# Performance work log

Measured on AMD Instinct MI355X. Metric: run time of the kernel, lower is better.

Reference implementation:

```python
import jax, jax.numpy as jnp
import numpy as np

Hh, Ww, Cc = 8, 8, 16        # observation grid h, w, channels
N = Hh * Ww                  # 64 graph nodes (one per grid cell)
B = 4096                     # batch
HEADS, COUT = 4, 32          # GAT heads, per-head output dim (concat -> 128)
HID, ADIM = 128, 6           # hidden_dim, action_dim
GAT_OUT = N * HEADS * COUT   # 8192 flattened GAT output per sample
NEG = -9e15


def _grid_adj():
    # 4-connected grid graph with self loops (make_graph's static edge structure)
    A = np.zeros((N, N), np.int32)
    for r in range(Hh):
        for c in range(Ww):
            i = r * Ww + c
            A[i, i] = 1
            for dr, dc in ((1, 0), (-1, 0), (0, 1), (0, -1)):
                rr, cc = r + dr, c + dc
                if 0 <= rr < Hh and 0 <= cc < Ww:
                    A[i, rr * Ww + cc] = 1
    return jnp.asarray(A)


def setup_inputs() -> dict:
    key = jax.random.key(0)
    ks = iter(jax.random.split(key, 40))
    p = lambda *s: jax.random.normal(next(ks), s, jnp.float32) * 0.1
    z = lambda *s: jnp.zeros(s, jnp.float32)
    return dict(
        x=jax.random.normal(next(ks), (B, Hh * Ww * Cc), jnp.float32),
        adj=_grid_adj(),
        actor_h=z(B, HID), actor_c=z(B, HID),
        critic_h=z(B, HID), critic_c=z(B, HID),
        gat1_W=p(Cc, HEADS * COUT), gat1_b=z(HEADS * COUT), gat1_a=p(HEADS, 2 * COUT),
        d1_W=p(GAT_OUT, HID), d1_b=z(HID),
        lstm1_Wi=p(HID, 4 * HID), lstm1_Wh=p(HID, 4 * HID), lstm1_b=z(4 * HID),
        ln1_s=jnp.ones((HID,), jnp.float32), ln1_bi=z(HID),
        d2_W=p(HID, HID), d2_b=z(HID),
        d3_W=p(HID, HID), d3_b=z(HID),
        dout_W=p(HID, ADIM), dout_b=z(ADIM),
        gat2_W=p(Cc, HEADS * COUT), gat2_b=z(HEADS * COUT), gat2_a=p(HEADS, 2 * COUT),
        c1_W=p(GAT_OUT, HID), c1_b=z(HID),
        lstm2_Wi=p(HID, 4 * HID), lstm2_Wh=p(HID, 4 * HID), lstm2_b=z(4 * HID),
        ln2_s=jnp.ones((HID,), jnp.float32), ln2_bi=z(HID),
        c2_W=p(HID, HID), c2_b=z(HID),
        c3_W=p(HID, HID), c3_b=z(HID),
        cout_W=p(HID, 1), cout_b=z(1),
    )


def _gat(feats, adj, W, b, a):
    # feats: [B,N,Cc]; adj: [N,N] int; multi-head GAT with concat heads
    h = (feats @ W + b).reshape(B, N, HEADS, COUT)           # [B,N,H,C]
    ls = jnp.einsum('bnhc,hc->bnh', h, a[:, :COUT])          # source logit
    ld = jnp.einsum('bnhc,hc->bnh', h, a[:, COUT:])          # dest logit
    logits = jax.nn.leaky_relu(ls[:, :, None, :] + ld[:, None, :, :], 0.2)  # [B,N,N,H]
    logits = jnp.where(adj[None, :, :, None] > 0, logits, NEG)
    attn = jax.nn.softmax(logits, axis=2)                    # over neighbors
    return jnp.einsum('bnmh,bmhc->bnhc', attn, h).reshape(B, -1)  # [B, N*H*C]


def _lstm(h, c, xin, Wi, Wh, bh):
    # flax OptimizedLSTMCell: gates in order i,f,g,o; bias only on hidden path
    z = xin @ Wi + h @ Wh + bh
    i, f, g, o = jnp.split(z, 4, axis=-1)
    nc = jax.nn.sigmoid(f) * c + jax.nn.sigmoid(i) * jnp.tanh(g)
    nh = jax.nn.sigmoid(o) * jnp.tanh(nc)
    return nh, nc


def _ln(v, s, b):
    mu = v.mean(-1, keepdims=True)
    var = v.var(-1, keepdims=True)
    return (v - mu) * jax.lax.rsqrt(var + 1e-6) * s + b


def reference(x, adj, actor_h, actor_c, critic_h, critic_c,
              gat1_W, gat1_b, gat1_a, d1_W, d1_b,
              lstm1_Wi, lstm1_Wh, lstm1_b, ln1_s, ln1_bi,
              d2_W, d2_b, d3_W, d3_b, dout_W, dout_b,
              gat2_W, gat2_b, gat2_a, c1_W, c1_b,
              lstm2_Wi, lstm2_Wh, lstm2_b, ln2_s, ln2_bi,
              c2_W, c2_b, c3_W, c3_b, cout_W, cout_b):
    act = jnp.tanh
    feats = x.reshape(B, N, Cc)
    # actor branch
    am = act(_gat(feats, adj, gat1_W, gat1_b, gat1_a) @ d1_W + d1_b)
    a_h, a_c = _lstm(actor_h, actor_c, am, lstm1_Wi, lstm1_Wh, lstm1_b)
    am = _ln(a_h, ln1_s, ln1_bi)
    am = act(am @ d2_W + d2_b)
    am = act(am @ d3_W + d3_b)
    logits = am @ dout_W + dout_b                            # Categorical logits
    # critic branch
    cm = act(_gat(feats, adj, gat2_W, gat2_b, gat2_a) @ c1_W + c1_b)
    c_h, c_c = _lstm(critic_h, critic_c, cm, lstm2_Wi, lstm2_Wh, lstm2_b)
    cm = _ln(c_h, ln2_s, ln2_bi)
    cm = act(cm @ c2_W + c2_b)
    cm = act(cm @ c3_W + c3_b)
    value = (cm @ cout_W + cout_b).squeeze(-1)
    return logits, value, a_h, a_c, c_h, c_c
```

## Files before the change

### kernel.cpp

```cpp
#include <hip/hip_runtime.h>
#include <hip/hip_bf16.h>

#define BATCH 4096
#define NN    64
#define CIN   16
#define NHEAD 4
#define CO    32
#define HC    128
#define HID   128
#define ADIM  6
#define K1    8192
#define LDH   136
#define KSPLIT 8

typedef __attribute__((ext_vector_type(8))) short bf16x8;
typedef __attribute__((ext_vector_type(8))) unsigned short u16x8;
typedef __attribute__((ext_vector_type(4))) float f32x4;

__device__ __forceinline__ float bf2f(unsigned short u) {
    unsigned int v = ((unsigned int)u) << 16;
    return __uint_as_float(v);
}
__device__ __forceinline__ unsigned short f2bf(float x) {
    union { __hip_bfloat16 h; unsigned short u; } cv;
    cv.h = __float2bfloat16(x);
    return cv.u;
}
__device__ __forceinline__ float sigmf(float x) { return 1.f / (1.f + expf(-x)); }

__device__ __forceinline__ void gload_lds16(const void* g, void* l) {
    __builtin_amdgcn_global_load_lds(
        (const __attribute__((address_space(1))) unsigned int*)(uintptr_t)g,
        (__attribute__((address_space(3))) unsigned int*)(uintptr_t)l,
        16, 0, 0);
}

struct TJob { const float* in; unsigned short* out; int K; int N; int ldo; };
struct TJobs { TJob j[8]; };

__global__ __launch_bounds__(256) void k_prep(
    const float* __restrict__ d1W, const float* __restrict__ c1W,
    unsigned short* __restrict__ Wt1, unsigned short* __restrict__ Wt2,
    TJobs jobs,
    const float* __restrict__ ha, const float* __restrict__ hc,
    unsigned short* __restrict__ X,
    const int* __restrict__ adj, unsigned long long* __restrict__ masks,
    const float* __restrict__ l1b, const float* __restrict__ l2b,
    const float* __restrict__ b2,  const float* __restrict__ c2b,
    const float* __restrict__ b3,  const float* __restrict__ c3b,
    float* __restrict__ biasz, float* __restrict__ b2p, float* __restrict__ b3p,
    const float* __restrict__ g1W, const float* __restrict__ g2W,
    const float* __restrict__ g1a, const float* __restrict__ g2a,
    const float* __restrict__ g1b, const float* __restrict__ g2b,
    unsigned short* __restrict__ wtg,
    float* __restrict__ blsld)
{
    const int bid = blockIdx.x;
    const int t   = threadIdx.x;

    if (bid < 1024) {
        __shared__ float s[64][33];
        const int  zsel = bid >> 9;
        const float* W  = zsel ? c1W : d1W;
        unsigned short* Wt = zsel ? Wt2 : Wt1;
        const int k0 = (bid & 127) * 64;
        const int n0 = ((bid >> 7) & 3) * 32;
        const int kr = t >> 5, nc = t & 31;
#pragma unroll
        for (int i = 0; i < 8; ++i)
            s[kr + 8 * i][nc] = W[(size_t)(k0 + kr + 8 * i) * HC + n0 + nc];
        __syncthreads();
#pragma unroll
        for (int j = 0; j < 8; ++j) {
            const int idx = j * 256 + t;
            const int n = idx >> 6, k = idx & 63;
            Wt[(size_t)(n0 + n) * K1 + k0 + k] = f2bf(s[k][n]);
        }
    } else if (bid < 1536) {
        const int b   = bid - 1024;
        const int job = b >> 6, idx = b & 63;
        const TJob jb = jobs.j[job];
        const int ntk = jb.K >> 5, ntn = jb.N >> 5;
        if (idx >= ntk * ntn) return;
        const int tk = idx % ntk, tn = idx / ntk;
        __shared__ float s2[32][33];
        const int kr = t >> 5, nc = t & 31;
        const int k0 = tk * 32, n0 = tn * 32;
#pragma unroll
        for (int i = 0; i < 4; ++i)
            s2[kr + 8 * i][nc] = jb.in[(size_t)(k0 + kr + 8 * i) * jb.N + n0 + nc];
        __syncthreads();
#pragma unroll
        for (int i = 0; i < 4; ++i) {
            const int idx2 = i * 256 + t;
            const int n = idx2 >> 5, k = idx2 & 31;
            jb.out[(size_t)(n0 + n) * jb.ldo + k0 + k] = f2bf(s2[k][n]);
        }
    } else if (bid < 2560) {
        const int gid = (bid - 1536) * 256 + t;
        const int zi  = gid >> 17;
        const int rem = gid & 131071;
        const int s3  = rem >> 5, c4 = rem & 31;
        const float4 v = reinterpret_cast<const float4*>(zi ? hc : ha)[(size_t)s3 * 32 + c4];
        ushort4 u;
        u.x = f2bf(v.x); u.y = f2bf(v.y); u.z = f2bf(v.z); u.w = f2bf(v.w);
        reinterpret_cast<ushort4*>(X + (size_t)zi * BATCH * 256 + (size_t)s3 * 256 + 128)[c4] = u;
    } else {
#pragma unroll
        for (int it = 0; it < 4; ++it) {
            const int tt = t + it * 256;
            if (tt < NN) {
                unsigned long long m = 0ull;
                for (int j = 0; j < NN; ++j)
                    if (adj[tt * NN + j] > 0) m |= (1ull << j);
                masks[tt] = m;
            }
            biasz[tt] = (tt < 512) ? l1b[tt] : l2b[tt - 512];
            if (tt < HID) {
                b2p[tt]       = b2[tt];
                b2p[HID + tt] = c2b[tt];
                b3p[tt]       = b3[tt];
                b3p[HID + tt] = c3b[tt];
            }
        }
#pragma unroll
        for (int q = 0; q < 16; ++q) {
            const int idx = t * 16 + q;
            const int set = idx >> 11;
            const int rem = idx & 2047;
            const int col = rem >> 4, k = rem & 15;
            wtg[set * 2304 + col * 16 + k] = f2bf((set ? g2W : g1W)[k * HC + col]);
        }
        {
            const int set = t >> 7, rem = t & 127;
            const int e = rem >> 4, k = rem & 15;
            const float* W  = set ? g2W : g1W;
            const float* aa = set ? g2a : g1a;
            const int hdh = e & 3, off = (e < 4) ? 0 : 32;
            float v = 0.f;
            for (int c = 0; c < 32; ++c)
                v += W[k * HC + hdh * 32 + c] * aa[hdh * 64 + off + c];
            wtg[set * 2304 + (128 + e) * 16 + k] = f2bf(v);
            wtg[set * 2304 + (136 + e) * 16 + k] = 0;
        }
        if (t < 16) {
            const int s2 = t >> 3, e2 = t & 7;
            const float* bb2 = s2 ? g2b : g1b;
            const float* aa2 = s2 ? g2a : g1a;
            const int h2 = e2 & 3, o2 = (e2 < 4) ? 0 : 32;
            float bv = 0.f;
            for (int c = 0; c < 32; ++c)
                bv += bb2[h2 * 32 + c] * aa2[h2 * 64 + o2 + c];
            blsld[s2 * 8 + e2] = bv;
        }
    }
}

struct GatW { const unsigned short* Wt; const float* b; const float* bls; unsigned short* out; };
struct GatArgs { GatW g[2]; };

__global__ __launch_bounds__(256) void k_gat(
    const float* __restrict__ x,
    const unsigned long long* __restrict__ masks,
    GatArgs ga, int zbase)
{
    const GatW gw = ga.g[zbase + blockIdx.y];
    const unsigned short* __restrict__ Wtg = gw.Wt;
    const float* __restrict__ bias = gw.b;
    const float* __restrict__ bls  = gw.bls;
    unsigned short* __restrict__ out = gw.out;

    union UB {
        struct { unsigned short feat[64][16]; unsigned short wt[144][16]; } stg;
        unsigned short P[2][64][72];
    };
    __shared__ UB u;
    __shared__ unsigned short s_hT[128][72];
    __shared__ float s_ls[64][4];
    __shared__ float s_ld[64][4];
    __shared__ float s_bias[HC];
    __shared__ float s_bls[8];
    __shared__ unsigned long long s_mask[NN];

    const int t = threadIdx.x;
    const int b = blockIdx.x;

    {
        const int n = t >> 2, c0 = (t & 3) * 4;
        const float4 v = reinterpret_cast<const float4*>(x + (size_t)b * (NN * CIN))[t];
        ushort4 q;
        q.x = f2bf(v.x); q.y = f2bf(v.y); q.z = f2bf(v.z); q.w = f2bf(v.w);
        *reinterpret_cast<ushort4*>(&u.stg.feat[n][c0]) = q;
        if (t < 144) {
            *reinterpret_cast<u16x8*>(&u.stg.wt[t][0]) = *reinterpret_cast<const u16x8*>(Wtg + t * 16);
            *reinterpret_cast<u16x8*>(&u.stg.wt[t][8]) = *reinterpret_cast<const u16x8*>(Wtg + t * 16 + 8);
        }
        if (t < HC) s_bias[t] = bias[t];
        if (t < 8)  s_bls[t] = bls[t];
        if (t < NN) s_mask[t] = masks[t];
    }
    __syncthreads();

    const int w = t >> 6, lane = t & 63;
    const int row16 = lane & 15;
    const int jr4   = lane >> 4;

    {
        const bool lo = lane < 32;
        const int k0 = (jr4 & 1) * 8;
        const bf16x8 zf = { 0, 0, 0, 0, 0, 0, 0, 0 };
        const bf16x8 aF = lo ? *reinterpret_cast<const bf16x8*>(&u.stg.feat[w * 16 + row16][k0]) : zf;
        bf16x8 bF[9];
#pragma unroll
        for (int ct = 0; ct < 9; ++ct)
            bF[ct] = lo ? *reinterpret_cast<const bf16x8*>(&u.stg.wt[ct * 16 + row16][k0]) : zf;
        f32x4 acc[9] = {};
#pragma unroll
        for (int ct = 0; ct < 9; ++ct)
            acc[ct] = __builtin_amdgcn_mfma_f32_16x16x32_bf16(aF, bF[ct], acc[ct], 0, 0, 0);
#pragma unroll
        for (int ct = 0; ct < 8; ++ct) {
            const int col = ct * 16 + row16;
            const float bv = s_bias[col];
            ushort4 q;
            q.x = f2bf(acc[ct][0] + bv);
            q.y = f2bf(acc[ct][1] + bv);
            q.z = f2bf(acc[ct][2] + bv);
            q.w = f2bf(acc[ct][3] + bv);
            *reinterpret_cast<ushort4*>(&s_hT[col][w * 16 + jr4 * 4]) = q;
        }
        if (row16 < 8) {
            const float bb = s_bls[row16];
#pragma unroll
            for (int j = 0; j < 4; ++j) {
                const int r = w * 16 + jr4 * 4 + j;
                if (row16 < 4) s_ls[r][row16]     = acc[8][j] + bb;
                else           s_ld[r][row16 - 4] = acc[8][j] + bb;
            }
        }
    }
    __syncthreads();

    const int n  = t >> 2;
    const int hd = t & 3;
    float p[5]; int mc[5]; bool ok[5];
    {
        const unsigned long long m = s_mask[n];
        const int cand[5] = { n - 8, n - 1, n, n + 1, n + 8 };
#pragma unroll
        for (int e = 0; e < 5; ++e) {
            const int cm = cand[e];
            const bool inr = (cm >= 0) && (cm < NN);
            mc[e] = inr ? cm : n;
            ok[e] = inr && ((m >> mc[e]) & 1ull);
        }
        const float lsn = s_ls[n][hd];
        float sum = 0.f;
#pragma unroll
        for (int e = 0; e < 5; ++e) {
            float v = lsn + s_ld[mc[e]][hd];
            v = (v > 0.f) ? v : 0.2f * v;
            p[e] = ok[e] ? __expf(v) : 0.f;
            sum += p[e];
        }
        const float inv = 1.f / sum;
#pragma unroll
        for (int e = 0; e < 5; ++e) p[e] *= inv;
    }

    {
        char* pb = (char*)&u.P[0][0][0];
#pragma unroll
        for (int i = 0; i < 9; ++i)
            *reinterpret_cast<unsigned long long*>(pb + t * 72 + i * 8) = 0ull;
    }
    __syncthreads();

    unsigned short* ob = out + (size_t)b * K1;

#pragma unroll
    for (int pass = 0; pass < 2; ++pass) {
        if ((hd >> 1) == pass) {
#pragma unroll
            for (int e = 0; e < 5; ++e)
                if (ok[e]) u.P[hd & 1][n][mc[e]] = f2bf(p[e]);
        }
        __syncthreads();

        const int hh  = pass * 2 + (w >> 1);
        const int ph  = w >> 1;
        const int mtb = (w & 1) * 2;
        f32x4 acc[2][2] = {};
#pragma unroll
        for (int kt = 0; kt < 2; ++kt) {
            const int kof = kt * 32 + jr4 * 8;
            bf16x8 aF[2], bF[2];
#pragma unroll
            for (int mtl = 0; mtl < 2; ++mtl)
                aF[mtl] = *reinterpret_cast<const bf16x8*>(&u.P[ph][(mtb + mtl) * 16 + row16][kof]);
#pragma unroll
            for (int nt = 0; nt < 2; ++nt)
                bF[nt] = *reinterpret_cast<const bf16x8*>(&s_hT[hh * 32 + nt * 16 + row16][kof]);
#pragma unroll
            for (int mtl = 0; mtl < 2; ++mtl)
#pragma unroll
                for (int nt = 0; nt < 2; ++nt)
                    acc[mtl][nt] = __builtin_amdgcn_mfma_f32_16x16x32_bf16(
                        aF[mtl], bF[nt], acc[mtl][nt], 0, 0, 0);
        }
#pragma unroll
        for (int mtl = 0; mtl < 2; ++mtl)
#pragma unroll
            for (int nt = 0; nt < 2; ++nt) {
                const int ch = hh * 32 + nt * 16 + row16;
#pragma unroll
                for (int j = 0; j < 4; ++j) {
                    const int node = (mtb + mtl) * 16 + jr4 * 4 + j;
                    ob[node * HC + ch] = f2bf(acc[mtl][nt][j]);
                }
            }
        if (pass == 0) __syncthreads();
    }
}

__global__ __launch_bounds__(256) void k_mmsk(
    const unsigned short* __restrict__ A0, const unsigned short* __restrict__ A1,
    const unsigned short* __restrict__ Bt0, const unsigned short* __restrict__ Bt1,
    float* __restrict__ accum)
{
    __shared__ unsigned short sbuf[2][160 * 64];

    const int br   = blockIdx.y;
    const unsigned short* A  = br ? A1 : A0;
    const unsigned short* Bt = br ? Bt1 : Bt0;
    float* acc_out = accum + (size_t)br * BATCH * HID;

    const int t    = threadIdx.x;
    const int w    = t >> 6;
    const int lane = t & 63;
    const int m0   = blockIdx.x * 32;
    const int kbase = blockIdx.z * (K1 / KSPLIT);
    const int kiters = (K1 / KSPLIT) / 64;

    const char* srcp[5];
    int ldsoff[5];
#pragma unroll
    for (int q = 0; q < 5; ++q) {
        const int c     = w * 5 + q;
        const int p     = c * 1024 + lane * 16;
        const int prow  = p >> 7;
        const int pslot = (p >> 4) & 7;
        const int lslot = pslot ^ (prow & 7);
        ldsoff[q] = c * 1024;
        if (c < 4)
            srcp[q] = (const char*)(A + (size_t)(m0 + prow) * K1 + kbase + lslot * 8);
        else
            srcp[q] = (const char*)(Bt + (size_t)(prow - 32) * K1 + kbase + lslot * 8);
    }

    f32x4 acc[2][2] = {};

#pragma unroll
    for (int q = 0; q < 5; ++q)
        gload_lds16(srcp[q], (char*)&sbuf[0][0] + ldsoff[q]);
    __syncthreads();

    int buf = 0;
    for (int it = 0; it < kiters; ++it) {
        if (it + 1 < kiters) {
            const size_t kbyte = (size_t)(it + 1) * 128;
#pragma unroll
            for (int q = 0; q < 5; ++q)
                gload_lds16(srcp[q] + kbyte, (char*)&sbuf[buf ^ 1][0] + ldsoff[q]);
        }
        const char* bb = (const char*)&sbuf[buf][0];
        bf16x8 aF[2][2], bF[2][2];
#pragma unroll
        for (int kb = 0; kb < 2; ++kb) {
            const int slot = kb * 4 + (lane >> 4);
#pragma unroll
            for (int rb = 0; rb < 2; ++rb) {
                const int row = rb * 16 + (lane & 15);
                aF[rb][kb] = *(const bf16x8*)(bb + row * 128 + ((slot ^ (row & 7)) << 4));
            }
#pragma unroll
            for (int cb = 0; cb < 2; ++cb) {
                const int row = 32 + w * 32 + cb * 16 + (lane & 15);
                bF[cb][kb] = *(const bf16x8*)(bb + row * 128 + ((slot ^ (row & 7)) << 4));
            }
        }
#pragma unroll
        for (int kb = 0; kb < 2; ++kb)
#pragma unroll
            for (int rb = 0; rb < 2; ++rb)
#pragma unroll
                for (int cb = 0; cb < 2; ++cb)
                    acc[rb][cb] = __builtin_amdgcn_mfma_f32_16x16x32_bf16(
                        aF[rb][kb], bF[cb][kb], acc[rb][cb], 0, 0, 0);
        __syncthreads();
        buf ^= 1;
    }

    const int col0 = w * 32;
    const int r0   = (lane >> 4) * 4;
    const int cc   = lane & 15;
#pragma unroll
    for (int rb = 0; rb < 2; ++rb)
#pragma unroll
        for (int cb = 0; cb < 2; ++cb) {
            const int col = col0 + cb * 16 + cc;
#pragma unroll
            for (int j = 0; j < 4; ++j) {
                const int row = m0 + rb * 16 + r0 + j;
                atomicAdd(&acc_out[(size_t)row * HID + col], acc[rb][cb][j]);
            }
        }
}

__global__ __launch_bounds__(256) void k_epi(
    const float* __restrict__ accum, const float* __restrict__ bias,
    unsigned short* __restrict__ Xo)
{
    const int gid = blockIdx.x * 256 + threadIdx.x;
    const int s = gid >> 5, c4 = gid & 31;
    const float4 v  = reinterpret_cast<const float4*>(accum)[gid];
    const float4 bv = reinterpret_cast<const float4*>(bias)[c4];
    ushort4 u;
    u.x = f2bf(tanhf(v.x + bv.x));
    u.y = f2bf(tanhf(v.y + bv.y));
    u.z = f2bf(tanhf(v.z + bv.z));
    u.w = f2bf(tanhf(v.w + bv.w));
    reinterpret_cast<ushort4*>(Xo + (size_t)s * 256)[c4] = u;
}

__global__ __launch_bounds__(256) void k_mm(
    const unsigned short* __restrict__ A, size_t aZ, int lda,
    const unsigned short* __restrict__ Bt, size_t bZ,
    const float* __restrict__ bias, size_t biasZ,
    float* __restrict__ outF, unsigned short* __restrict__ outB,
    size_t oZ, int ldo, int kiters, int act)
{
    __shared__ unsigned short sbuf[2][160 * 64];

    const int t    = threadIdx.x;
    const int w    = t >> 6;
    const int lane = t & 63;
    const int m0   = blockIdx.x * 32;
    const int n0   = blockIdx.y * 128;
    const int z    = blockIdx.z;
    const int K    = kiters * 64;

    const unsigned short* Az = A  + (size_t)z * aZ;
    const unsigned short* Bz = Bt + (size_t)z * bZ + (size_t)n0 * K;

    const char* srcp[5];
    int ldsoff[5];
#pragma unroll
    for (int q = 0; q < 5; ++q) {
        const int c     = w * 5 + q;
        const int p     = c * 1024 + lane * 16;
        const int prow  = p >> 7;
        const int pslot = (p >> 4) & 7;
        const int lslot = pslot ^ (prow & 7);
        ldsoff[q] = c * 1024;
        if (c < 4)
            srcp[q] = (const char*)(Az + (size_t)(m0 + prow) * lda + lslot * 8);
        else
            srcp[q] = (const char*)(Bz + (size_t)(prow - 32) * K + lslot * 8);
    }

    f32x4 acc[2][2] = {};

#pragma unroll
    for (int q = 0; q < 5; ++q)
        gload_lds16(srcp[q], (char*)&sbuf[0][0] + ldsoff[q]);
    __syncthreads();

    int buf = 0;
    for (int it = 0; it < kiters; ++it) {
        if (it + 1 < kiters) {
            const size_t kbyte = (size_t)(it + 1) * 128;
#pragma unroll
            for (int q = 0; q < 5; ++q)
                gload_lds16(srcp[q] + kbyte, (char*)&sbuf[buf ^ 1][0] + ldsoff[q]);
        }
        const char* bb = (const char*)&sbuf[buf][0];
        bf16x8 aF[2][2], bF[2][2];
#pragma unroll
        for (int kb = 0; kb < 2; ++kb) {
            const int slot = kb * 4 + (lane >> 4);
#pragma unroll
            for (int rb = 0; rb < 2; ++rb) {
                const int row = rb * 16 + (lane & 15);
                aF[rb][kb] = *(const bf16x8*)(bb + row * 128 + ((slot ^ (row & 7)) << 4));
            }
#pragma unroll
            for (int cb = 0; cb < 2; ++cb) {
                const int row = 32 + w * 32 + cb * 16 + (lane & 15);
                bF[cb][kb] = *(const bf16x8*)(bb + row * 128 + ((slot ^ (row & 7)) << 4));
            }
        }
#pragma unroll
        for (int kb = 0; kb < 2; ++kb)
#pragma unroll
            for (int rb = 0; rb < 2; ++rb)
#pragma unroll
                for (int cb = 0; cb < 2; ++cb)
                    acc[rb][cb] = __builtin_amdgcn_mfma_f32_16x16x32_bf16(
                        aF[rb][kb], bF[cb][kb], acc[rb][cb], 0, 0, 0);
        __syncthreads();
        buf ^= 1;
    }

    const int col0 = w * 32;
    const int r0   = (lane >> 4) * 4;
    const int cc   = lane & 15;
#pragma unroll
    for (int rb = 0; rb < 2; ++rb)
#pragma unroll
        for (int cb = 0; cb < 2; ++cb) {
            const int col = col0 + cb * 16 + cc;
            const float bv = bias ? bias[(size_t)z * biasZ + n0 + col] : 0.f;
#pragma unroll
            for (int j = 0; j < 4; ++j) {
                const int row = m0 + rb * 16 + r0 + j;
                float v = acc[rb][cb][j] + bv;
                if (act) v = tanhf(v);
                const size_t off = (size_t)z * oZ + (size_t)row * ldo + n0 + col;
                if (outB) outB[off] = f2bf(v);
                else      outF[off] = v;
            }
        }
}

__global__ __launch_bounds__(256) void k_tail(
    const float* __restrict__ zbuf,
    const float* __restrict__ c0a, const float* __restrict__ c0c,
    const float* __restrict__ sA,  const float* __restrict__ bA,
    const float* __restrict__ sC,  const float* __restrict__ bC,
    const unsigned short* __restrict__ W23t,
    const float* __restrict__ b2p, const float* __restrict__ b3p,
    const float* __restrict__ doW, const float* __restrict__ dob,
    const float* __restrict__ coW, const float* __restrict__ cob,
    float* __restrict__ hA, float* __restrict__ cA,
    float* __restrict__ hC, float* __restrict__ cC,
    float* __restrict__ logits, float* __restrict__ value)
{
    __shared__ unsigned short s_ln[32][LDH];
    __shared__ unsigned short s_t2[32][LDH];
    __shared__ unsigned short s_t3[32][LDH];
    __shared__ unsigned short s_w[128][LDH];

    const int t  = threadIdx.x;
    const int zi = blockIdx.y;
    const int s0 = blockIdx.x * 32;

    const unsigned short* W2 = W23t + (size_t)zi * HID * HID;
    const unsigned short* W3 = W23t + (size_t)(2 + zi) * HID * HID;

    {
        const int s  = t >> 3, l8 = t & 7;
        const int gb = s0 + s;
        const float* zr  = zbuf + (size_t)zi * BATCH * 512 + (size_t)gb * 512;
        const float* c0  = (zi ? c0c : c0a) + (size_t)gb * HID;
        float* oh = (zi ? hC : hA) + (size_t)gb * HID;
        float* oc = (zi ? cC : cA) + (size_t)gb * HID;
        const float* lns = zi ? sC : sA;
        const float* lnb = zi ? bC : bA;
        const int u0 = l8 * 16;

        float nh16[16];
        float sum = 0.f, sumsq = 0.f;
#pragma unroll
        for (int r4 = 0; r4 < 4; ++r4) {
            const int u = u0 + r4 * 4;
            const float4 gi = *reinterpret_cast<const float4*>(&zr[u]);
            const float4 gf = *reinterpret_cast<const float4*>(&zr[128 + u]);
            const float4 gg = *reinterpret_cast<const float4*>(&zr[256 + u]);
            const float4 go = *reinterpret_cast<const float4*>(&zr[384 + u]);
            const float4 cv = *reinterpret_cast<const float4*>(&c0[u]);
            float4 ncv, nhv;
            ncv.x = sigmf(gf.x) * cv.x + sigmf(gi.x) * tanhf(gg.x);
            ncv.y = sigmf(gf.y) * cv.y + sigmf(gi.y) * tanhf(gg.y);
            ncv.z = sigmf(gf.z) * cv.z + sigmf(gi.z) * tanhf(gg.z);
            ncv.w = sigmf(gf.w) * cv.w + sigmf(gi.w) * tanhf(gg.w);
            nhv.x = sigmf(go.x) * tanhf(ncv.x);
            nhv.y = sigmf(go.y) * tanhf(ncv.y);
            nhv.z = sigmf(go.z) * tanhf(ncv.z);
            nhv.w = sigmf(go.w) * tanhf(ncv.w);
            *reinterpret_cast<float4*>(&oc[u]) = ncv;
            *reinterpret_cast<float4*>(&oh[u]) = nhv;
            nh16[r4 * 4 + 0] = nhv.x; nh16[r4 * 4 + 1] = nhv.y;
            nh16[r4 * 4 + 2] = nhv.z; nh16[r4 * 4 + 3] = nhv.w;
            sum   += nhv.x + nhv.y + nhv.z + nhv.w;
            sumsq += nhv.x * nhv.x + nhv.y * nhv.y + nhv.z * nhv.z + nhv.w * nhv.w;
        }
        for (int msk = 1; msk < 8; msk <<= 1) {
            sum   += __shfl_xor(sum, msk, 8);
            sumsq += __shfl_xor(sumsq, msk, 8);
        }
        const float mu   = sum * (1.f / 128.f);
        const float var  = sumsq * (1.f / 128.f) - mu * mu;
        const float rstd = rsqrtf(var + 1e-6f);
        u16x8 lo, hi;
#pragma unroll
        for (int r = 0; r < 8; ++r) {
            lo[r] = f2bf((nh16[r] - mu) * rstd * lns[u0 + r] + lnb[u0 + r]);
            hi[r] = f2bf((nh16[8 + r] - mu) * rstd * lns[u0 + 8 + r] + lnb[u0 + 8 + r]);
        }
        *reinterpret_cast<u16x8*>(&s_ln[s][u0])     = lo;
        *reinterpret_cast<u16x8*>(&s_ln[s][u0 + 8]) = hi;

        const int col = t >> 1, half = (t & 1) * 64;
#pragma unroll
        for (int q = 0; q < 8; ++q) {
            const u16x8 wv = *reinterpret_cast<const u16x8*>(W2 + col * HID + half + q * 8);
            *reinterpret_cast<u16x8*>(&s_w[col][half + q * 8]) = wv;
        }
    }
    __syncthreads();

    const int w = t >> 6, lane = t & 63;
    const int row16 = lane & 15, k08 = (lane >> 4) * 8;

    {
        f32x4 acc[2][2] = {};
#pragma unroll
        for (int ks = 0; ks < 4; ++ks) {
            bf16x8 aF[2], bF[2];
#pragma unroll
            for (int rt = 0; rt < 2; ++rt)
                aF[rt] = *reinterpret_cast<const bf16x8*>(&s_ln[rt * 16 + row16][ks * 32 + k08]);
#pragma unroll
            for (int ct = 0; ct < 2; ++ct)
                bF[ct] = *reinterpret_cast<const bf16x8*>(&s_w[w * 32 + ct * 16 + row16][ks * 32 + k08]);
#pragma unroll
            for (int rt = 0; rt < 2; ++rt)
#pragma unroll
                for (int ct = 0; ct < 2; ++ct)
                    acc[rt][ct] = __builtin_amdgcn_mfma_f32_16x16x32_bf16(
                        aF[rt], bF[ct], acc[rt][ct], 0, 0, 0);
        }
#pragma unroll
        for (int rt = 0; rt < 2; ++rt)
#pragma unroll
            for (int ct = 0; ct < 2; ++ct) {
                const int col = w * 32 + ct * 16 + row16;
                const float bv = b2p[zi * HID + col];
#pragma unroll
                for (int j = 0; j < 4; ++j)
                    s_t2[rt * 16 + (lane >> 4) * 4 + j][col] = f2bf(tanhf(acc[rt][ct][j] + bv));
            }
    }
    __syncthreads();

    {
        const int col = t >> 1, half = (t & 1) * 64;
#pragma unroll
        for (int q = 0; q < 8; ++q) {
            const u16x8 wv = *reinterpret_cast<const u16x8*>(W3 + col * HID + half + q * 8);
            *reinterpret_cast<u16x8*>(&s_w[col][half + q * 8]) = wv;
        }
    }
    __syncthreads();

    {
        f32x4 acc[2][2] = {};
#pragma unroll
        for (int ks = 0; ks < 4; ++ks) {
            bf16x8 aF[2], bF[2];
#pragma unroll
            for (int rt = 0; rt < 2; ++rt)
                aF[rt] = *reinterpret_cast<const bf16x8*>(&s_t2[rt * 16 + row16][ks * 32 + k08]);
#pragma unroll
            for (int ct = 0; ct < 2; ++ct)
                bF[ct] = *reinterpret_cast<const bf16x8*>(&s_w[w * 32 + ct * 16 + row16][ks * 32 + k08]);
#pragma unroll
            for (int rt = 0; rt < 2; ++rt)
#pragma unroll
                for (int ct = 0; ct < 2; ++ct)
                    acc[rt][ct] = __builtin_amdgcn_mfma_f32_16x16x32_bf16(
                        aF[rt], bF[ct], acc[rt][ct], 0, 0, 0);
        }
#pragma unroll
        for (int rt = 0; rt < 2; ++rt)
#pragma unroll
            for (int ct = 0; ct < 2; ++ct) {
                const int col = w * 32 + ct * 16 + row16;
                const float bv = b3p[zi * HID + col];
#pragma unroll
                for (int j = 0; j < 4; ++j)
                    s_t3[rt * 16 + (lane >> 4) * 4 + j][col] = f2bf(tanhf(acc[rt][ct][j] + bv));
            }
    }
    __syncthreads();

    if (zi == 0) {
        if (t < 32 * ADIM) {
            const int s = t / ADIM, a2 = t % ADIM;
            float acc = dob[a2];
            for (int k = 0; k < HID; ++k)
                acc = fmaf(bf2f(s_t3[s][k]), doW[k * ADIM + a2], acc);
            logits[(size_t)(s0 + s) * ADIM + a2] = acc;
        }
    } else {
        if (t < 32) {
            float acc = cob[0];
            for (int k = 0; k < HID; ++k)
                acc = fmaf(bf2f(s_t3[t][k]), coW[k], acc);
            value[s0 + t] = acc;
        }
    }
}

extern "C" void kernel_launch(void* const* d_in, const int* in_sizes, int n_in,
                              void* d_out, int out_size, void* d_ws, size_t ws_size,
                              hipStream_t stream)
{
    (void)in_sizes; (void)n_in; (void)out_size;

    const float* x        = (const float*)d_in[0];
    const int*   adj      = (const int*)  d_in[1];
    const float* actor_h  = (const float*)d_in[2];
    const float* actor_c  = (const float*)d_in[3];
    const float* critic_h = (const float*)d_in[4];
    const float* critic_c = (const float*)d_in[5];
    const float* gat1_W   = (const float*)d_in[6];
    const float* gat1_b   = (const float*)d_in[7];
    const float* gat1_a   = (const float*)d_in[8];
    const float* d1_W     = (const float*)d_in[9];
    const float* d1_b     = (const float*)d_in[10];
    const float* l1_Wi    = (const float*)d_in[11];
    const float* l1_Wh    = (const float*)d_in[12];
    const float* l1_b     = (const float*)d_in[13];
    const float* ln1_s    = (const float*)d_in[14];
    const float* ln1_b    = (const float*)d_in[15];
    const float* d2_W     = (const float*)d_in[16];
    const float* d2_b     = (const float*)d_in[17];
    const float* d3_W     = (const float*)d_in[18];
    const float* d3_b     = (const float*)d_in[19];
    const float* dout_W   = (const float*)d_in[20];
    const float* dout_b   = (const float*)d_in[21];
    const float* gat2_W   = (const float*)d_in[22];
    const float* gat2_b   = (const float*)d_in[23];
    const float* gat2_a   = (const float*)d_in[24];
    const float* c1_W     = (const float*)d_in[25];
    const float* c1_b     = (const float*)d_in[26];
    const float* l2_Wi    = (const float*)d_in[27];
    const float* l2_Wh    = (const float*)d_in[28];
    const float* l2_b     = (const float*)d_in[29];
    const float* ln2_s    = (const float*)d_in[30];
    const float* ln2_b    = (const float*)d_in[31];
    const float* c2_W     = (const float*)d_in[32];
    const float* c2_b     = (const float*)d_in[33];
    const float* c3_W     = (const float*)d_in[34];
    const float* c3_b     = (const float*)d_in[35];
    const float* cout_W   = (const float*)d_in[36];
    const float* cout_b   = (const float*)d_in[37];

    float* out      = (float*)d_out;
    float* o_logits = out;
    float* o_value  = out + (size_t)BATCH * ADIM;
    float* o_ah     = o_value + BATCH;
    float* o_ac     = o_ah + (size_t)BATCH * HID;
    float* o_ch     = o_ac + (size_t)BATCH * HID;
    float* o_cc     = o_ch + (size_t)BATCH * HID;

    char* ws = (char*)d_ws;
    const size_t MB = 1024 * 1024;
    const size_t KB = 1024;
    unsigned long long* masks = (unsigned long long*)ws;
    float* bias_z = (float*)(ws + 4 * KB);
    float* b2p    = (float*)(ws + 8 * KB);
    float* b3p    = (float*)(ws + 12 * KB);
    unsigned short* wtg = (unsigned short*)(ws + 16 * KB);
    float* blsld  = (float*)(ws + 60 * KB);
    float* accum  = (float*)(ws + 64 * KB);
    unsigned short* Wt1  = (unsigned short*)(ws + 64 * KB + 4 * MB);
    unsigned short* Wt2  = (unsigned short*)(ws + 64 * KB + 6 * MB);
    unsigned short* Wcat = (unsigned short*)(ws + 64 * KB + 8 * MB);
    unsigned short* W23t = (unsigned short*)(ws + 64 * KB + 8 * MB + 512 * KB);
    unsigned short* X    = (unsigned short*)(ws + 64 * KB + 8 * MB + 768 * KB);
    const size_t off_big = 64 * KB + 8 * MB + 768 * KB + 4 * MB;
    char* big = ws + off_big;
    unsigned short* gatA = (unsigned short*)big;
    const bool dual = ws_size >= off_big + 128 * MB;
    unsigned short* gatB = dual ? (unsigned short*)(big + 64 * MB) : gatA;
    float*          zbuf = (float*)big;

    TJobs tj;
    tj.j[0] = { l1_Wi, Wcat,                        HID, 512, 256 };
    tj.j[1] = { l1_Wh, Wcat + 128,                  HID, 512, 256 };
    tj.j[2] = { l2_Wi, Wcat + 512 * 256,            HID, 512, 256 };
    tj.j[3] = { l2_Wh, Wcat + 512 * 256 + 128,      HID, 512, 256 };
    tj.j[4] = { d2_W,  W23t,                        HID, HID, HID };
    tj.j[5] = { c2_W,  W23t + 128 * 128,            HID, HID, HID };
    tj.j[6] = { d3_W,  W23t + 2 * 128 * 128,        HID, HID, HID };
    tj.j[7] = { c3_W,  W23t + 3 * 128 * 128,        HID, HID, HID };
    hipLaunchKernelGGL(k_prep, dim3(2561), dim3(256), 0, stream,
                       d1_W, c1_W, Wt1, Wt2, tj,
                       actor_h, critic_h, X,
                       adj, masks, l1_b, l2_b, d2_b, c2_b, d3_b, c3_b,
                       bias_z, b2p, b3p, gat1_W, gat2_W,
                       gat1_a, gat2_a, gat1_b, gat2_b, wtg, blsld);

    GatArgs ga;
    ga.g[0] = { wtg,        gat1_b, blsld,     gatA };
    ga.g[1] = { wtg + 2304, gat2_b, blsld + 8, gatB };

    if (dual) {
        hipMemsetAsync(accum, 0, (size_t)2 * BATCH * HID * 4, stream);
        hipLaunchKernelGGL(k_gat, dim3(BATCH, 2), dim3(256), 0, stream,
                           x, masks, ga, 0);
        hipLaunchKernelGGL(k_mmsk, dim3(BATCH / 32, 2, KSPLIT), dim3(256), 0, stream,
                           gatA, gatB, Wt1, Wt2, accum);
        hipLaunchKernelGGL(k_epi, dim3(512), dim3(256), 0, stream,
                           accum, d1_b, X);
        hipLaunchKernelGGL(k_epi, dim3(512), dim3(256), 0, stream,
                           accum + (size_t)BATCH * HID, c1_b, X + (size_t)BATCH * 256);
    } else {
        hipLaunchKernelGGL(k_gat, dim3(BATCH, 1), dim3(256), 0, stream,
                           x, masks, ga, 0);
        hipMemsetAsync(accum, 0, (size_t)BATCH * HID * 4, stream);
        hipLaunchKernelGGL(k_mmsk, dim3(BATCH / 32, 1, KSPLIT), dim3(256), 0, stream,
                           gatA, gatA, Wt1, Wt1, accum);
        hipLaunchKernelGGL(k_epi, dim3(512), dim3(256), 0, stream,
                           accum, d1_b, X);
        hipLaunchKernelGGL(k_gat, dim3(BATCH, 1), dim3(256), 0, stream,
                           x, masks, ga, 1);
        hipMemsetAsync(accum, 0, (size_t)BATCH * HID * 4, stream);
        hipLaunchKernelGGL(k_mmsk, dim3(BATCH / 32, 1, KSPLIT), dim3(256), 0, stream,
                           gatA, gatA, Wt2, Wt2, accum);
        hipLaunchKernelGGL(k_epi, dim3(512), dim3(256), 0, stream,
                           accum, c1_b, X + (size_t)BATCH * 256);
    }

    hipLaunchKernelGGL(k_mm, dim3(BATCH / 32, 4, 2), dim3(256), 0, stream,
                       X, (size_t)BATCH * 256, 256, Wcat, (size_t)512 * 256,
                       bias_z, (size_t)512,
                       zbuf, (unsigned short*)nullptr, (size_t)BATCH * 512, 512, 4, 0);

    hipLaunchKernelGGL(k_tail, dim3(BATCH / 32, 2), dim3(256), 0, stream,
                       zbuf, actor_c, critic_c, ln1_s, ln1_b, ln2_s, ln2_b,
                       W23t, b2p, b3p, dout_W, dout_b, cout_W, cout_b,
                       o_ah, o_ac, o_ch, o_cc, o_logits, o_value);
}
```

Measured before the change: 135.9 us.

## Stage GAT output through LDS in channel-major layout with vectorized stores

The GAT kernel now keeps both passes' MFMA accumulators in registers, writes them transposed into a shared-memory tile, and stores each sample's output as contiguous 16-byte chunks in channel-major order. Before, it issued scattered 2-byte global stores. The weight-transpose prep kernel permutes the rows of the dense-layer weights to match the new output layout, so the downstream GEMM consumes it unchanged. This trades more register pressure and an extra LDS round trip for coalesced global writes.

```diff
diff --git a/kernel.cpp b/kernel.cpp
--- a/kernel.cpp
+++ b/kernel.cpp
@@ -65,10 +65,13 @@
         unsigned short* Wt = zsel ? Wt2 : Wt1;
         const int k0 = (bid & 127) * 64;
         const int n0 = ((bid >> 7) & 3) * 32;
+        const int ch = k0 >> 6;
         const int kr = t >> 5, nc = t & 31;
 #pragma unroll
-        for (int i = 0; i < 8; ++i)
-            s[kr + 8 * i][nc] = W[(size_t)(k0 + kr + 8 * i) * HC + n0 + nc];
+        for (int i = 0; i < 8; ++i) {
+            const int kk = kr + 8 * i;
+            s[kk][nc] = W[(size_t)(kk * HC + ch) * HC + n0 + nc];
+        }
         __syncthreads();
 #pragma unroll
         for (int j = 0; j < 8; ++j) {
@@ -173,6 +176,7 @@
     union UB {
         struct { unsigned short feat[64][16]; unsigned short wt[144][16]; } stg;
         unsigned short P[2][64][72];
+        unsigned short outS[128][72];
     };
     __shared__ UB u;
     __shared__ unsigned short s_hT[128][72];
@@ -276,7 +280,7 @@
     }
     __syncthreads();
 
-    unsigned short* ob = out + (size_t)b * K1;
+    f32x4 accO[2][2][2];
 
 #pragma unroll
     for (int pass = 0; pass < 2; ++pass) {
@@ -290,7 +294,11 @@
         const int hh  = pass * 2 + (w >> 1);
         const int ph  = w >> 1;
         const int mtb = (w & 1) * 2;
-        f32x4 acc[2][2] = {};
+#pragma unroll
+        for (int mtl = 0; mtl < 2; ++mtl)
+#pragma unroll
+            for (int nt = 0; nt < 2; ++nt)
+                accO[pass][mtl][nt] = f32x4{ 0.f, 0.f, 0.f, 0.f };
 #pragma unroll
         for (int kt = 0; kt < 2; ++kt) {
             const int kof = kt * 32 + jr4 * 8;
@@ -305,21 +313,42 @@
             for (int mtl = 0; mtl < 2; ++mtl)
 #pragma unroll
                 for (int nt = 0; nt < 2; ++nt)
-                    acc[mtl][nt] = __builtin_amdgcn_mfma_f32_16x16x32_bf16(
-                        aF[mtl], bF[nt], acc[mtl][nt], 0, 0, 0);
-        }
-#pragma unroll
-        for (int mtl = 0; mtl < 2; ++mtl)
-#pragma unroll
-            for (int nt = 0; nt < 2; ++nt) {
-                const int ch = hh * 32 + nt * 16 + row16;
-#pragma unroll
-                for (int j = 0; j < 4; ++j) {
-                    const int node = (mtb + mtl) * 16 + jr4 * 4 + j;
-                    ob[node * HC + ch] = f2bf(acc[mtl][nt][j]);
+                    accO[pass][mtl][nt] = __builtin_amdgcn_mfma_f32_16x16x32_bf16(
+                        aF[mtl], bF[nt], accO[pass][mtl][nt], 0, 0, 0);
+        }
+        __syncthreads();
+    }
+
+    {
+        const int mtb = (w & 1) * 2;
+#pragma unroll
+        for (int pass = 0; pass < 2; ++pass) {
+            const int hh = pass * 2 + (w >> 1);
+#pragma unroll
+            for (int mtl = 0; mtl < 2; ++mtl)
+#pragma unroll
+                for (int nt = 0; nt < 2; ++nt) {
+                    const int ch = hh * 32 + nt * 16 + row16;
+                    const int n0 = (mtb + mtl) * 16 + jr4 * 4;
+                    ushort4 q;
+                    q.x = f2bf(accO[pass][mtl][nt][0]);
+                    q.y = f2bf(accO[pass][mtl][nt][1]);
+                    q.z = f2bf(accO[pass][mtl][nt][2]);
+                    q.w = f2bf(accO[pass][mtl][nt][3]);
+                    *reinterpret_cast<ushort4*>(&u.outS[ch][n0]) = q;
                 }
-            }
-        if (pass == 0) __syncthreads();
+        }
+    }
+    __syncthreads();
+
+    {
+        unsigned short* ob = out + (size_t)b * K1;
+        const int ch = t >> 1, half = (t & 1) * 32;
+#pragma unroll
+        for (int k = 0; k < 4; ++k) {
+            const u16x8 v = *reinterpret_cast<const u16x8*>(&u.outS[ch][half + k * 8]);
+            *reinterpret_cast<u16x8*>(ob + ch * 64 + half + k * 8) = v;
+        }
     }
 }
 
```

Result: slower. 158.3 us (+16.5%).
